# Optimization experiments

Hardware: AMD Instinct MI355X
Metric: run time of the kernel (lower is better)

The kernel has to match this reference:

```python
import jax, jax.numpy as jnp
import numpy as np

M = 7
NUM_HEADS = 4
DIM = 128
HD = DIM // NUM_HEADS
SCALE = HD ** -0.5
B_WIN = 4096
N = M * M


def _relative_position_bias_index(m):
    # Faithful numpy replica of the torch index construction (meshgrid 'ij').
    ii, jj = np.meshgrid(np.arange(m), np.arange(m), indexing='ij')
    coords = np.stack([ii, jj]).reshape(2, -1)                  # (2, M*M)
    rel = coords[:, :, None] - coords[:, None, :]               # (2, MM, MM)
    rel = rel.transpose(1, 2, 0)                                # (MM, MM, 2)
    rel = rel + (m - 1)
    rel[:, :, 0] += 2 * m - 1
    return rel.sum(2).astype(np.int32)                          # (MM, MM)


def setup_inputs() -> dict:
    key = jax.random.key(0)
    ks = jax.random.split(key, 6)
    s = 0.02
    return {
        'x': jax.random.normal(ks[0], (B_WIN, N, DIM), jnp.float32),
        'qkv_w': jax.random.normal(ks[1], (DIM, 3 * DIM), jnp.float32) * s,
        'qkv_b': jnp.zeros((3 * DIM,), jnp.float32),
        'wo_w': jax.random.normal(ks[2], (DIM, DIM), jnp.float32) * s,
        'wo_b': jnp.zeros((DIM,), jnp.float32),
        'bias_table': jax.random.normal(ks[3], ((2 * (M - 1)) ** 2, NUM_HEADS), jnp.float32) * s,
        'bias_index': jnp.asarray(_relative_position_bias_index(M)),
    }


def reference(x, qkv_w, qkv_b, wo_w, wo_b, bias_table, bias_index):
    B, n, d = x.shape
    qkv = x @ qkv_w + qkv_b                                     # (B, n, 3d)
    qkv = qkv.reshape(B, n, 3, NUM_HEADS, HD).transpose(2, 0, 3, 1, 4)  # (3,B,H,n,hd)
    Q, K, V = qkv[0], qkv[1], qkv[2]
    # relative position bias: (n, n, H) -> (1, H, n, n)
    bias = bias_table[bias_index].transpose(2, 0, 1)[None]
    scores = jnp.einsum('bhqd,bhkd->bhqk', Q, K) * SCALE + bias
    attn = jax.nn.softmax(scores, axis=-1)
    out = jnp.einsum('bhqk,bhkd->bhqd', attn, V)                # (B,H,n,hd)
    out = out.transpose(0, 2, 1, 3).reshape(B, n, d)
    return out @ wo_w + wo_b
```

## Files before the change

### kernel.cpp

```cpp
#include <hip/hip_runtime.h>
#include <cstdint>

namespace {
constexpr int NWIN = 4096;
constexpr int NT   = 49;
constexpr int D    = 128;
constexpr float SCALE = 0.17677669529663687f;

constexpr int SQ = 136;
constexpr int SV = 72;

constexpr size_t WQH   = 0;
constexpr size_t WOH   = 49152;
constexpr size_t WOL   = 65536;
constexpr size_t BFRAG = 81920;
constexpr size_t WBUF_BYTES = 98304 * 2;

constexpr size_t VSCR_OFF_USH = 98304;
constexpr size_t TOTAL_WS_BYTES = WBUF_BYTES + (size_t)NWIN * 8192 * 2;
}

using short8 = __attribute__((ext_vector_type(8))) short;
using f32x4  = __attribute__((ext_vector_type(4))) float;

__device__ __forceinline__ ushort f2bf(float x) {
    uint u = __builtin_bit_cast(uint, x);
    uint r = u + 0x7FFFu + ((u >> 16) & 1u);
    return (ushort)(r >> 16);
}
__device__ __forceinline__ ushort f2bf_tr(float x) {
    return (ushort)(__builtin_bit_cast(uint, x) >> 16);
}
__device__ __forceinline__ float bf2f(ushort b) {
    uint u = ((uint)b) << 16;
    return __builtin_bit_cast(float, u);
}
__device__ __forceinline__ uint pack_bf2(float a, float b) {
    return ((uint)f2bf(a)) | (((uint)f2bf(b)) << 16);
}

__global__ __launch_bounds__(256) void prep_all(
    const float* __restrict__ qkv_w, const float* __restrict__ wo_w,
    const float* __restrict__ bias_table, const int* __restrict__ bias_index,
    ushort* __restrict__ wbuf)
{
    const int blk = blockIdx.x, tid = threadIdx.x;
    if (blk < 96) {
        const int nt = blk >> 2, ks = blk & 3;
        for (int e = tid; e < 512; e += 256) {
            const int lane = e >> 3, j = e & 7;
            const int k = ks * 32 + (lane >> 4) * 8 + j;
            const int n = nt * 16 + (lane & 15);
            float wv = qkv_w[(size_t)k * 384 + n];
            if (n < 128) wv *= SCALE;
            wbuf[WQH + ((size_t)(nt * 4 + ks) * 64 + lane) * 8 + j] = f2bf(wv);
        }
    } else if (blk < 128) {
        const int b2 = blk - 96;
        const int nt = b2 >> 2, ks = b2 & 3;
        for (int e = tid; e < 512; e += 256) {
            const int lane = e >> 3, j = e & 7;
            const int k = ks * 32 + (lane >> 4) * 8 + j;
            const int n = nt * 16 + (lane & 15);
            const float wv = wo_w[(size_t)k * 128 + n];
            const ushort h = f2bf(wv);
            const size_t fo = ((size_t)(nt * 4 + ks) * 64 + lane) * 8 + j;
            wbuf[WOH + fo] = h;
            wbuf[WOL + fo] = f2bf(wv - bf2f(h));
        }
    } else {
        const int p = blk - 128;
        const int h = p >> 2, qt = p & 3;
        for (int ei = tid; ei < 1024; ei += 256) {
            const int lane = ei >> 4, t = (ei >> 2) & 3, r = ei & 3;
            const int q = qt * 16 + (lane & 15);
            const int k = 16 * t + 4 * (lane >> 4) + r;
            float v = 0.f;
            if (q < NT && k < NT) v = bias_table[bias_index[q * NT + k] * 4 + h];
            wbuf[BFRAG + (size_t)p * 1024 + ei] = f2bf(v);
        }
    }
}

__global__ __launch_bounds__(512, 4) void win2_fused(
    const float* __restrict__ x, const float* __restrict__ qkv_b,
    const ushort* __restrict__ wbuf, const float* __restrict__ wo_b,
    ushort* __restrict__ vscr, float* __restrict__ out)
{
    __shared__ __align__(16) ushort s_q[2][64 * SQ];
    __shared__ __align__(16) ushort s_k[2][64 * SQ];

    const int b = blockIdx.x, tid = threadIdx.x;
    const int wid = tid >> 6, lane = tid & 63;
    const int g = lane >> 4, lr = lane & 15;

    const int m = wid >> 1;
    const int nt0 = (wid & 1) * 12;

    short8 Ax[2][4];
    {
        const int row = m * 16 + lr;
        #pragma unroll
        for (int wi = 0; wi < 2; ++wi) {
            if (row < NT) {
                const float* xr = x + (size_t)(b * 2 + wi) * NT * D + row * D;
                #pragma unroll
                for (int ks = 0; ks < 4; ++ks) {
                    const float4 v0 = *reinterpret_cast<const float4*>(&xr[ks * 32 + g * 8]);
                    const float4 v1 = *reinterpret_cast<const float4*>(&xr[ks * 32 + g * 8 + 4]);
                    uint4 w;
                    w.x = pack_bf2(v0.x, v0.y); w.y = pack_bf2(v0.z, v0.w);
                    w.z = pack_bf2(v1.x, v1.y); w.w = pack_bf2(v1.z, v1.w);
                    Ax[wi][ks] = __builtin_bit_cast(short8, w);
                }
            } else {
                #pragma unroll
                for (int ks = 0; ks < 4; ++ks) Ax[wi][ks] = short8{0,0,0,0,0,0,0,0};
            }
        }
    }
    float qb[12];
    #pragma unroll
    for (int i = 0; i < 12; ++i) {
        const int nt = nt0 + i;
        float v = qkv_b[nt * 16 + lr];
        if (nt < 8) v *= SCALE;
        qb[i] = v;
    }

    #pragma unroll
    for (int pass = 0; pass < 4; ++pass) {
        const int ntb = nt0 + pass * 3;
        f32x4 acc[2][3] = {};
        #pragma unroll
        for (int ks = 0; ks < 4; ++ks) {
            short8 Bf[3];
            #pragma unroll
            for (int i = 0; i < 3; ++i)
                Bf[i] = *reinterpret_cast<const short8*>(
                    &wbuf[WQH + ((size_t)((ntb + i) * 4 + ks) * 64 + lane) * 8]);
            #pragma unroll
            for (int i = 0; i < 3; ++i) {
                acc[0][i] = __builtin_amdgcn_mfma_f32_16x16x32_bf16(Ax[0][ks], Bf[i], acc[0][i], 0, 0, 0);
                acc[1][i] = __builtin_amdgcn_mfma_f32_16x16x32_bf16(Ax[1][ks], Bf[i], acc[1][i], 0, 0, 0);
            }
        }
        #pragma unroll
        for (int i = 0; i < 3; ++i) {
            const int nt = ntb + i;
            const int n = nt * 16 + lr;
            const float bias = qb[pass * 3 + i];
            #pragma unroll
            for (int wi = 0; wi < 2; ++wi) {
                if (nt < 16) {
                    ushort* const dst = (nt < 8) ? &s_q[wi][0] : &s_k[wi][0];
                    const int col = n & 127;
                    #pragma unroll
                    for (int jj = 0; jj < 4; ++jj)
                        dst[(m * 16 + g * 4 + jj) * SQ + col] = f2bf_tr(acc[wi][i][jj] + bias);
                } else {
                    const int d  = n - 256;
                    const int f  = ((d >> 5) * 2 + ((d >> 4) & 1)) * 2 + (m >> 1);
                    const int j0 = 4 * (m & 1);
                    ushort4 hv;
                    #pragma unroll
                    for (int jj = 0; jj < 4; ++jj)
                        (&hv.x)[jj] = f2bf(acc[wi][i][jj] + bias);
                    ushort* const vw = vscr + (size_t)(b * 2 + wi) * 8192;
                    *reinterpret_cast<ushort4*>(&vw[((size_t)f * 64 + lane) * 8 + j0]) = hv;
                }
            }
        }
    }
    __syncthreads();

    const int wi3 = wid >> 2;
    const int h   = wid & 3;
    const ushort* const vwp = vscr + (size_t)(b * 2 + wi3) * 8192;
    f32x4 oac[4][2];
    {
        short8 Vf[2][2];
        #pragma unroll
        for (int dt = 0; dt < 2; ++dt)
            #pragma unroll
            for (int ks = 0; ks < 2; ++ks)
                Vf[dt][ks] = *reinterpret_cast<const short8*>(
                    &vwp[((size_t)(((h * 2 + dt) * 2) + ks) * 64 + lane) * 8]);

        #pragma unroll
        for (int pi = 0; pi < 4; ++pi) {
            const int qt = pi;
            const int p  = h * 4 + qt;
            const short8 Qf = *reinterpret_cast<const short8*>(&s_q[wi3][(qt * 16 + lr) * SQ + h * 32 + g * 8]);
            f32x4 sc[4];
            #pragma unroll
            for (int t = 0; t < 4; ++t) {
                const short8 Kf = *reinterpret_cast<const short8*>(&s_k[wi3][(t * 16 + lr) * SQ + h * 32 + g * 8]);
                f32x4 z = {};
                sc[t] = __builtin_amdgcn_mfma_f32_16x16x32_bf16(Kf, Qf, z, 0, 0, 0);
            }
            uint bw[8];
            {
                const uint4 b0 = *reinterpret_cast<const uint4*>(&wbuf[BFRAG + ((size_t)p * 64 + lane) * 16]);
                const uint4 b1 = *reinterpret_cast<const uint4*>(&wbuf[BFRAG + ((size_t)p * 64 + lane) * 16 + 8]);
                bw[0] = b0.x; bw[1] = b0.y; bw[2] = b0.z; bw[3] = b0.w;
                bw[4] = b1.x; bw[5] = b1.y; bw[6] = b1.z; bw[7] = b1.w;
            }
            float ev[16];
            float lsum = 0.f;
            #pragma unroll
            for (int t = 0; t < 4; ++t) {
                #pragma unroll
                for (int r = 0; r < 4; ++r) {
                    const int idx = 4 * t + r;
                    const uint bwv = bw[idx >> 1];
                    const float bv = __builtin_bit_cast(float, (idx & 1) ? (bwv & 0xFFFF0000u) : (bwv << 16));
                    float e;
                    if (t < 3) {
                        e = __expf(sc[t][r] + bv);
                    } else if (r == 0) {
                        e = (g == 0) ? __expf(sc[t][0] + bv) : 0.f;
                    } else {
                        e = 0.f;
                    }
                    ev[idx] = e;
                    lsum += e;
                }
            }
            lsum += __shfl_xor(lsum, 16);
            lsum += __shfl_xor(lsum, 32);
            const float inv = 1.f / lsum;
            uint pw[8];
            #pragma unroll
            for (int i = 0; i < 8; ++i)
                pw[i] = pack_bf2(ev[2 * i] * inv, ev[2 * i + 1] * inv);
            uint4 w0, w1;
            w0.x = pw[0]; w0.y = pw[1]; w0.z = pw[2]; w0.w = pw[3];
            w1.x = pw[4]; w1.y = pw[5]; w1.z = pw[6]; w1.w = pw[7];
            const short8 pa0 = __builtin_bit_cast(short8, w0);
            const short8 pa1 = __builtin_bit_cast(short8, w1);
            #pragma unroll
            for (int dt = 0; dt < 2; ++dt) {
                f32x4 o = {};
                o = __builtin_amdgcn_mfma_f32_16x16x32_bf16(pa0, Vf[dt][0], o, 0, 0, 0);
                o = __builtin_amdgcn_mfma_f32_16x16x32_bf16(pa1, Vf[dt][1], o, 0, 0, 0);
                oac[pi][dt] = o;
            }
        }
    }
    __syncthreads();

    #pragma unroll
    for (int pi = 0; pi < 4; ++pi) {
        #pragma unroll
        for (int dt = 0; dt < 2; ++dt) {
            const int d = h * 32 + dt * 16 + lr;
            #pragma unroll
            for (int r = 0; r < 4; ++r) {
                const int q = pi * 16 + 4 * g + r;
                s_q[wi3][q * SQ + d] = f2bf(oac[pi][dt][r]);
            }
        }
    }
    __syncthreads();

    {
        const int wi4 = wid >> 2;
        const int ntp = wid & 3;
        float wb2[2];
        wb2[0] = wo_b[ntp * 16 + lr];
        wb2[1] = wo_b[(ntp + 4) * 16 + lr];
        f32x4 acc[2][4] = {};
        #pragma unroll
        for (int ks = 0; ks < 4; ++ks) {
            short8 Ah[4];
            #pragma unroll
            for (int mm = 0; mm < 4; ++mm)
                Ah[mm] = *reinterpret_cast<const short8*>(&s_q[wi4][(mm * 16 + lr) * SQ + ks * 32 + g * 8]);
            #pragma unroll
            for (int i = 0; i < 2; ++i) {
                const int nt = ntp + i * 4;
                const size_t fo = ((size_t)(nt * 4 + ks) * 64 + lane) * 8;
                const short8 Wh = *reinterpret_cast<const short8*>(&wbuf[WOH + fo]);
                const short8 Wl = *reinterpret_cast<const short8*>(&wbuf[WOL + fo]);
                #pragma unroll
                for (int mm = 0; mm < 4; ++mm) {
                    acc[i][mm] = __builtin_amdgcn_mfma_f32_16x16x32_bf16(Ah[mm], Wh, acc[i][mm], 0, 0, 0);
                    acc[i][mm] = __builtin_amdgcn_mfma_f32_16x16x32_bf16(Ah[mm], Wl, acc[i][mm], 0, 0, 0);
                }
            }
        }
        float* ob = out + (size_t)(b * 2 + wi4) * NT * D;
        #pragma unroll
        for (int i = 0; i < 2; ++i) {
            const int n = (ntp + i * 4) * 16 + lr;
            #pragma unroll
            for (int mm = 0; mm < 4; ++mm) {
                #pragma unroll
                for (int jj = 0; jj < 4; ++jj) {
                    const int q = mm * 16 + 4 * g + jj;
                    if (q < NT) ob[q * D + n] = acc[i][mm][jj] + wb2[i];
                }
            }
        }
    }
}

__global__ __launch_bounds__(512, 4) void win_attn_np(
    const float* __restrict__ x,
    const float* __restrict__ qkv_w, const float* __restrict__ qkv_b,
    const float* __restrict__ wo_w,  const float* __restrict__ wo_b,
    const float* __restrict__ bias_table, const int* __restrict__ bias_index,
    float* __restrict__ out)
{
    __shared__ __align__(16) ushort s_all[26624];
    ushort* const s_qh = s_all;
    ushort* const s_kh = s_all + 8704;
    ushort* const s_vt = s_all + 17408;

    const int b = blockIdx.x, tid = threadIdx.x;
    const int wid = tid >> 6, lane = tid & 63;
    const int g = lane >> 4, lr = lane & 15;
    const int m = wid >> 1;
    const int nt0 = (wid & 1) * 12;
    const float* xb = x + (size_t)b * NT * D;

    short8 Ax[4];
    {
        const int row = m * 16 + lr;
        if (row < NT) {
            const float* xr = xb + row * D;
            #pragma unroll
            for (int ks = 0; ks < 4; ++ks) {
                const float4 v0 = *reinterpret_cast<const float4*>(&xr[ks * 32 + g * 8]);
                const float4 v1 = *reinterpret_cast<const float4*>(&xr[ks * 32 + g * 8 + 4]);
                uint4 w;
                w.x = pack_bf2(v0.x, v0.y); w.y = pack_bf2(v0.z, v0.w);
                w.z = pack_bf2(v1.x, v1.y); w.w = pack_bf2(v1.z, v1.w);
                Ax[ks] = __builtin_bit_cast(short8, w);
            }
        } else {
            #pragma unroll
            for (int ks = 0; ks < 4; ++ks) Ax[ks] = short8{0,0,0,0,0,0,0,0};
        }
    }
    float qb[12];
    #pragma unroll
    for (int i = 0; i < 12; ++i) {
        const int nt = nt0 + i;
        float v = qkv_b[nt * 16 + lr];
        if (nt < 8) v *= SCALE;
        qb[i] = v;
    }

    #pragma unroll
    for (int pass = 0; pass < 2; ++pass) {
        const int ntb = nt0 + pass * 6;
        f32x4 acc[6] = {};
        #pragma unroll
        for (int ks = 0; ks < 4; ++ks) {
            short8 Bf[6];
            #pragma unroll
            for (int i = 0; i < 6; ++i) {
                #pragma unroll
                for (int j = 0; j < 8; ++j) {
                    float wv = qkv_w[(size_t)(ks * 32 + g * 8 + j) * 384 + (ntb + i) * 16 + lr];
                    if (ntb + i < 8) wv *= SCALE;
                    Bf[i][j] = (short)f2bf(wv);
                }
            }
            #pragma unroll
            for (int i = 0; i < 6; ++i)
                acc[i] = __builtin_amdgcn_mfma_f32_16x16x32_bf16(Ax[ks], Bf[i], acc[i], 0, 0, 0);
        }
        #pragma unroll
        for (int i = 0; i < 6; ++i) {
            const int nt = ntb + i;
            const int n = nt * 16 + lr;
            const float bias = qb[pass * 6 + i];
            if (nt < 16) {
                ushort* const dst = (nt < 8) ? s_qh : s_kh;
                const int col = n & 127;
                #pragma unroll
                for (int jj = 0; jj < 4; ++jj) {
                    const int q = m * 16 + g * 4 + jj;
                    dst[q * SQ + col] = f2bf_tr(acc[i][jj] + bias);
                }
            } else {
                const int d = n - 256;
                const int cbase = 32 * (m >> 1) + 8 * ((4 * m + g) & 3) + 4 * (m & 1);
                ushort4 hv;
                #pragma unroll
                for (int jj = 0; jj < 4; ++jj)
                    (&hv.x)[jj] = f2bf(acc[i][jj] + bias);
                *reinterpret_cast<ushort4*>(&s_vt[d * SV + cbase]) = hv;
            }
        }
    }
    __syncthreads();

    {
        short8 pa[2][2];
        float inv2[2];
        #pragma unroll
        for (int pi = 0; pi < 2; ++pi) {
            const int p = wid * 2 + pi;
            const int h = p >> 2, qt = p & 3;
            uint bw[8];
            {
                const int q = qt * 16 + lr;
                #pragma unroll
                for (int t = 0; t < 4; ++t) {
                    #pragma unroll
                    for (int r = 0; r < 4; r += 2) {
                        const int k0 = 16 * t + 4 * g + r, k1 = k0 + 1;
                        float v0 = 0.f, v1 = 0.f;
                        if (q < NT && k0 < NT) v0 = bias_table[bias_index[q * NT + k0] * 4 + h];
                        if (q < NT && k1 < NT) v1 = bias_table[bias_index[q * NT + k1] * 4 + h];
                        bw[(4 * t + r) >> 1] = ((uint)f2bf(v0)) | (((uint)f2bf(v1)) << 16);
                    }
                }
            }
            const short8 Qf = *reinterpret_cast<const short8*>(&s_qh[(qt * 16 + lr) * SQ + h * 32 + g * 8]);
            f32x4 sc[4];
            #pragma unroll
            for (int t = 0; t < 4; ++t) {
                const short8 Kf = *reinterpret_cast<const short8*>(&s_kh[(t * 16 + lr) * SQ + h * 32 + g * 8]);
                f32x4 z = {};
                sc[t] = __builtin_amdgcn_mfma_f32_16x16x32_bf16(Kf, Qf, z, 0, 0, 0);
            }
            float lsum = 0.f;
            uint pw[8];
            #pragma unroll
            for (int t = 0; t < 4; ++t) {
                float ebits[4];
                #pragma unroll
                for (int r = 0; r < 4; ++r) {
                    const int idx = 4 * t + r;
                    const uint bwv = bw[idx >> 1];
                    const float bv = __builtin_bit_cast(float, (idx & 1) ? (bwv & 0xFFFF0000u) : (bwv << 16));
                    float e;
                    if (t < 3) {
                        e = __expf(sc[t][r] + bv);
                    } else if (r == 0) {
                        e = (g == 0) ? __expf(sc[t][0] + bv) : 0.f;
                    } else {
                        e = 0.f;
                    }
                    const uint tr = __builtin_bit_cast(uint, e) & 0xFFFF0000u;
                    ebits[r] = __builtin_bit_cast(float, tr);
                    lsum += ebits[r];
                }
                pw[t * 2 + 0] = (__builtin_bit_cast(uint, ebits[0]) >> 16) | (__builtin_bit_cast(uint, ebits[1]) & 0xFFFF0000u);
                pw[t * 2 + 1] = (__builtin_bit_cast(uint, ebits[2]) >> 16) | (__builtin_bit_cast(uint, ebits[3]) & 0xFFFF0000u);
            }
            lsum += __shfl_xor(lsum, 16);
            lsum += __shfl_xor(lsum, 32);
            inv2[pi] = 1.f / lsum;
            #pragma unroll
            for (int ks = 0; ks < 2; ++ks) {
                uint4 w;
                w.x = pw[(2 * ks) * 2 + 0]; w.y = pw[(2 * ks) * 2 + 1];
                w.z = pw[(2 * ks + 1) * 2 + 0]; w.w = pw[(2 * ks + 1) * 2 + 1];
                pa[pi][ks] = __builtin_bit_cast(short8, w);
            }
        }

        f32x4 oac[2][2];
        #pragma unroll
        for (int pi = 0; pi < 2; ++pi) {
            const int p = wid * 2 + pi;
            const int h = p >> 2;
            #pragma unroll
            for (int dt = 0; dt < 2; ++dt) {
                f32x4 o = {};
                #pragma unroll
                for (int ks = 0; ks < 2; ++ks) {
                    const short8 Vf = *reinterpret_cast<const short8*>(&s_vt[(h * 32 + dt * 16 + lr) * SV + ks * 32 + g * 8]);
                    o = __builtin_amdgcn_mfma_f32_16x16x32_bf16(pa[pi][ks], Vf, o, 0, 0, 0);
                }
                oac[pi][dt] = o;
            }
        }
        __syncthreads();

        #pragma unroll
        for (int pi = 0; pi < 2; ++pi) {
            const int p = wid * 2 + pi;
            const int h = p >> 2, qt = p & 3;
            #pragma unroll
            for (int dt = 0; dt < 2; ++dt) {
                const int d = h * 32 + dt * 16 + lr;
                #pragma unroll
                for (int r = 0; r < 4; ++r) {
                    const float inv = __shfl(inv2[pi], 4 * g + r);
                    const int q = qt * 16 + 4 * g + r;
                    s_qh[q * SQ + d] = f2bf(oac[pi][dt][r] * inv);
                }
            }
        }
    }
    __syncthreads();

    {
        const int nt04 = (wid & 1) * 4;
        float wb4[4];
        #pragma unroll
        for (int i = 0; i < 4; ++i) wb4[i] = wo_b[(nt04 + i) * 16 + lr];
        f32x4 acc[4] = {};
        #pragma unroll
        for (int ks = 0; ks < 4; ++ks) {
            short8 Wh[4], Wl[4];
            #pragma unroll
            for (int i = 0; i < 4; ++i) {
                #pragma unroll
                for (int j = 0; j < 8; ++j) {
                    const float wv = wo_w[(size_t)(ks * 32 + g * 8 + j) * 128 + (nt04 + i) * 16 + lr];
                    const ushort hh = f2bf(wv);
                    Wh[i][j] = (short)hh;
                    Wl[i][j] = (short)f2bf(wv - bf2f(hh));
                }
            }
            const short8 Ah = *reinterpret_cast<const short8*>(&s_qh[(m * 16 + lr) * SQ + ks * 32 + g * 8]);
            #pragma unroll
            for (int i = 0; i < 4; ++i) {
                acc[i] = __builtin_amdgcn_mfma_f32_16x16x32_bf16(Ah, Wh[i], acc[i], 0, 0, 0);
                acc[i] = __builtin_amdgcn_mfma_f32_16x16x32_bf16(Ah, Wl[i], acc[i], 0, 0, 0);
            }
        }
        float* ob = out + (size_t)b * NT * D;
        #pragma unroll
        for (int i = 0; i < 4; ++i) {
            const int n = (nt04 + i) * 16 + lr;
            #pragma unroll
            for (int jj = 0; jj < 4; ++jj) {
                const int q = m * 16 + g * 4 + jj;
                if (q < NT) ob[q * D + n] = acc[i][jj] + wb4[i];
            }
        }
    }
}

extern "C" void kernel_launch(void* const* d_in, const int* in_sizes, int n_in,
                              void* d_out, int out_size, void* d_ws, size_t ws_size,
                              hipStream_t stream) {
    const float* x          = (const float*)d_in[0];
    const float* qkv_w      = (const float*)d_in[1];
    const float* qkv_b      = (const float*)d_in[2];
    const float* wo_w       = (const float*)d_in[3];
    const float* wo_b       = (const float*)d_in[4];
    const float* bias_table = (const float*)d_in[5];
    const int*   bias_index = (const int*)d_in[6];
    float* outp = (float*)d_out;

    if (ws_size >= TOTAL_WS_BYTES) {
        ushort* wbuf = (ushort*)d_ws;
        ushort* vscr = wbuf + VSCR_OFF_USH;
        prep_all<<<dim3(144), dim3(256), 0, stream>>>(qkv_w, wo_w, bias_table, bias_index, wbuf);
        win2_fused<<<dim3(NWIN / 2), dim3(512), 0, stream>>>(x, qkv_b, wbuf, wo_b, vscr, outp);
    } else {
        win_attn_np<<<dim3(NWIN), dim3(512), 0, stream>>>(
            x, qkv_w, qkv_b, wo_w, wo_b, bias_table, bias_index, outp);
    }
}
```

Measured before the change: 108.9 us.

## Repartition warp work in QKV and output projections to cut weight fragment loads

```diff
diff --git a/kernel.cpp b/kernel.cpp
--- a/kernel.cpp
+++ b/kernel.cpp
@@ -94,14 +94,15 @@
     const int wid = tid >> 6, lane = tid & 63;
     const int g = lane >> 4, lr = lane & 15;
 
-    const int m = wid >> 1;
-    const int nt0 = (wid & 1) * 12;
-
-    short8 Ax[2][4];
-    {
-        const int row = m * 16 + lr;
-        #pragma unroll
-        for (int wi = 0; wi < 2; ++wi) {
+    const int mp  = wid >> 2;
+    const int nt0 = (wid & 3) * 6;
+
+    short8 Ax[2][2][4];
+    #pragma unroll
+    for (int wi = 0; wi < 2; ++wi) {
+        #pragma unroll
+        for (int mi = 0; mi < 2; ++mi) {
+            const int row = (2 * mp + mi) * 16 + lr;
             if (row < NT) {
                 const float* xr = x + (size_t)(b * 2 + wi) * NT * D + row * D;
                 #pragma unroll
@@ -111,17 +112,17 @@
                     uint4 w;
                     w.x = pack_bf2(v0.x, v0.y); w.y = pack_bf2(v0.z, v0.w);
                     w.z = pack_bf2(v1.x, v1.y); w.w = pack_bf2(v1.z, v1.w);
-                    Ax[wi][ks] = __builtin_bit_cast(short8, w);
+                    Ax[wi][mi][ks] = __builtin_bit_cast(short8, w);
                 }
             } else {
                 #pragma unroll
-                for (int ks = 0; ks < 4; ++ks) Ax[wi][ks] = short8{0,0,0,0,0,0,0,0};
-            }
-        }
-    }
-    float qb[12];
+                for (int ks = 0; ks < 4; ++ks) Ax[wi][mi][ks] = short8{0,0,0,0,0,0,0,0};
+            }
+        }
+    }
+    float qb[6];
     #pragma unroll
-    for (int i = 0; i < 12; ++i) {
+    for (int i = 0; i < 6; ++i) {
         const int nt = nt0 + i;
         float v = qkv_b[nt * 16 + lr];
         if (nt < 8) v *= SCALE;
@@ -129,35 +130,35 @@
     }
 
     #pragma unroll
-    for (int pass = 0; pass < 4; ++pass) {
-        const int ntb = nt0 + pass * 3;
-        f32x4 acc[2][3] = {};
+    for (int i = 0; i < 6; ++i) {
+        const int nt = nt0 + i;
+        short8 Bf[4];
+        #pragma unroll
+        for (int ks = 0; ks < 4; ++ks)
+            Bf[ks] = *reinterpret_cast<const short8*>(
+                &wbuf[WQH + ((size_t)(nt * 4 + ks) * 64 + lane) * 8]);
+        f32x4 acc[2][2] = {};
         #pragma unroll
         for (int ks = 0; ks < 4; ++ks) {
-            short8 Bf[3];
-            #pragma unroll
-            for (int i = 0; i < 3; ++i)
-                Bf[i] = *reinterpret_cast<const short8*>(
-                    &wbuf[WQH + ((size_t)((ntb + i) * 4 + ks) * 64 + lane) * 8]);
-            #pragma unroll
-            for (int i = 0; i < 3; ++i) {
-                acc[0][i] = __builtin_amdgcn_mfma_f32_16x16x32_bf16(Ax[0][ks], Bf[i], acc[0][i], 0, 0, 0);
-                acc[1][i] = __builtin_amdgcn_mfma_f32_16x16x32_bf16(Ax[1][ks], Bf[i], acc[1][i], 0, 0, 0);
-            }
-        }
-        #pragma unroll
-        for (int i = 0; i < 3; ++i) {
-            const int nt = ntb + i;
-            const int n = nt * 16 + lr;
-            const float bias = qb[pass * 3 + i];
             #pragma unroll
             for (int wi = 0; wi < 2; ++wi) {
+                acc[wi][0] = __builtin_amdgcn_mfma_f32_16x16x32_bf16(Ax[wi][0][ks], Bf[ks], acc[wi][0], 0, 0, 0);
+                acc[wi][1] = __builtin_amdgcn_mfma_f32_16x16x32_bf16(Ax[wi][1][ks], Bf[ks], acc[wi][1], 0, 0, 0);
+            }
+        }
+        const int n = nt * 16 + lr;
+        const float bias = qb[i];
+        #pragma unroll
+        for (int wi = 0; wi < 2; ++wi) {
+            #pragma unroll
+            for (int mi = 0; mi < 2; ++mi) {
+                const int m = 2 * mp + mi;
                 if (nt < 16) {
                     ushort* const dst = (nt < 8) ? &s_q[wi][0] : &s_k[wi][0];
                     const int col = n & 127;
                     #pragma unroll
                     for (int jj = 0; jj < 4; ++jj)
-                        dst[(m * 16 + g * 4 + jj) * SQ + col] = f2bf_tr(acc[wi][i][jj] + bias);
+                        dst[(m * 16 + g * 4 + jj) * SQ + col] = f2bf_tr(acc[wi][mi][jj] + bias);
                 } else {
                     const int d  = n - 256;
                     const int f  = ((d >> 5) * 2 + ((d >> 4) & 1)) * 2 + (m >> 1);
@@ -165,7 +166,7 @@
                     ushort4 hv;
                     #pragma unroll
                     for (int jj = 0; jj < 4; ++jj)
-                        (&hv.x)[jj] = f2bf(acc[wi][i][jj] + bias);
+                        (&hv.x)[jj] = f2bf(acc[wi][mi][jj] + bias);
                     ushort* const vw = vscr + (size_t)(b * 2 + wi) * 8192;
                     *reinterpret_cast<ushort4*>(&vw[((size_t)f * 64 + lane) * 8 + j0]) = hv;
                 }
@@ -265,41 +266,35 @@
     __syncthreads();
 
     {
-        const int wi4 = wid >> 2;
-        const int ntp = wid & 3;
-        float wb2[2];
-        wb2[0] = wo_b[ntp * 16 + lr];
-        wb2[1] = wo_b[(ntp + 4) * 16 + lr];
+        const int nt = wid;
+        const float wb = wo_b[nt * 16 + lr];
         f32x4 acc[2][4] = {};
         #pragma unroll
         for (int ks = 0; ks < 4; ++ks) {
-            short8 Ah[4];
-            #pragma unroll
-            for (int mm = 0; mm < 4; ++mm)
-                Ah[mm] = *reinterpret_cast<const short8*>(&s_q[wi4][(mm * 16 + lr) * SQ + ks * 32 + g * 8]);
-            #pragma unroll
-            for (int i = 0; i < 2; ++i) {
-                const int nt = ntp + i * 4;
-                const size_t fo = ((size_t)(nt * 4 + ks) * 64 + lane) * 8;
-                const short8 Wh = *reinterpret_cast<const short8*>(&wbuf[WOH + fo]);
-                const short8 Wl = *reinterpret_cast<const short8*>(&wbuf[WOL + fo]);
+            const size_t fo = ((size_t)(nt * 4 + ks) * 64 + lane) * 8;
+            const short8 Wh = *reinterpret_cast<const short8*>(&wbuf[WOH + fo]);
+            const short8 Wl = *reinterpret_cast<const short8*>(&wbuf[WOL + fo]);
+            #pragma unroll
+            for (int wi = 0; wi < 2; ++wi) {
                 #pragma unroll
                 for (int mm = 0; mm < 4; ++mm) {
-                    acc[i][mm] = __builtin_amdgcn_mfma_f32_16x16x32_bf16(Ah[mm], Wh, acc[i][mm], 0, 0, 0);
-                    acc[i][mm] = __builtin_amdgcn_mfma_f32_16x16x32_bf16(Ah[mm], Wl, acc[i][mm], 0, 0, 0);
-                }
-            }
-        }
-        float* ob = out + (size_t)(b * 2 + wi4) * NT * D;
-        #pragma unroll
-        for (int i = 0; i < 2; ++i) {
-            const int n = (ntp + i * 4) * 16 + lr;
+                    const short8 Ah = *reinterpret_cast<const short8*>(
+                        &s_q[wi][(mm * 16 + lr) * SQ + ks * 32 + g * 8]);
+                    acc[wi][mm] = __builtin_amdgcn_mfma_f32_16x16x32_bf16(Ah, Wh, acc[wi][mm], 0, 0, 0);
+                    acc[wi][mm] = __builtin_amdgcn_mfma_f32_16x16x32_bf16(Ah, Wl, acc[wi][mm], 0, 0, 0);
+                }
+            }
+        }
+        #pragma unroll
+        for (int wi = 0; wi < 2; ++wi) {
+            float* ob = out + (size_t)(b * 2 + wi) * NT * D;
+            const int n = nt * 16 + lr;
             #pragma unroll
             for (int mm = 0; mm < 4; ++mm) {
                 #pragma unroll
                 for (int jj = 0; jj < 4; ++jj) {
                     const int q = mm * 16 + 4 * g + jj;
-                    if (q < NT) ob[q * D + n] = acc[i][mm][jj] + wb2[i];
+                    if (q < NT) ob[q * D + n] = acc[wi][mm][jj] + wb;
                 }
             }
         }
```

After: 117.6 us. 1.08x slower.
